# Optimization experiments

Hardware: AMD Instinct MI355X
Metric: run time of the kernel (lower is better)

The kernel has to match this reference:

```python
import jax, jax.numpy as jnp
import numpy as np

N, E, B = 20000, 320000, 64   # nodes, edges, graphs
H, L = 32, 3                  # hidden dim (dim_inner), message passes
HH = H * H
IDX = jnp.array([[0, 1, 2, 3, 4, 5],
                 [1, 6, 7, 8, 9, 10],
                 [2, 7, 11, 12, 13, 14],
                 [3, 8, 12, 15, 16, 17],
                 [4, 9, 13, 16, 18, 19],
                 [5, 10, 14, 17, 19, 20]])


def setup_inputs() -> dict:
    key = jax.random.key(0)
    ks = iter(jax.random.split(key, 40))
    def nrm(shape, s=0.1):
        return jax.random.normal(next(ks), shape, jnp.float32) * s
    inp = {}
    inp['node_attrs'] = jax.random.normal(next(ks), (N, 1), jnp.float32)
    inp['positions'] = jax.random.normal(next(ks), (N, 3), jnp.float32)
    inp['shifts'] = jax.random.normal(next(ks), (E, 3), jnp.float32) * 0.01
    inp['edge_attr'] = jax.random.uniform(next(ks), (E, 1), jnp.float32)
    inp['edge_index'] = jax.random.randint(next(ks), (2, E), 0, N)
    inp['batch_ids'] = jax.random.randint(next(ks), (N,), 0, B)
    # node embedding Linear(1, H)
    inp['embed_W'] = nrm((1, H), 1.0)
    inp['embed_b'] = nrm((H,))
    # per-layer edge MLP: 5 -> H -> H -> H*H (all with bias), plus NNConv bias
    inp['e_W1'] = nrm((L, 5, H), 0.4)
    inp['e_b1'] = nrm((L, H))
    inp['e_W2'] = nrm((L, H, H), 0.15)
    inp['e_b2'] = nrm((L, H))
    inp['e_W3'] = nrm((L, H, HH), 0.15)
    inp['e_b3'] = nrm((L, HH))
    inp['conv_b'] = nrm((L, H))
    # head MLP: H -> 128 -> 64 -> 32 -> 21
    inp['h_W1'] = nrm((H, 128), 0.15)
    inp['h_b1'] = nrm((128,))
    inp['h_W2'] = nrm((128, 64), 0.1)
    inp['h_b2'] = nrm((64,))
    inp['h_W3'] = nrm((64, 32), 0.12)
    inp['h_b3'] = nrm((32,))
    inp['h_W4'] = nrm((32, 21), 0.18)
    inp['h_b4'] = nrm((21,))
    return inp


def reference(node_attrs, positions, shifts, edge_attr, edge_index, batch_ids,
              embed_W, embed_b, e_W1, e_b1, e_W2, e_b2, e_W3, e_b3, conv_b,
              h_W1, h_b1, h_W2, h_b2, h_W3, h_b3, h_W4, h_b4):
    src, dst = edge_index[0], edge_index[1]
    x = node_attrs @ embed_W + embed_b                       # [N, H]
    # get_edge_vectors_and_lengths (MACE convention): receiver - sender + shifts
    vec = positions[dst] - positions[src] + shifts            # [E, 3]
    length = jnp.linalg.norm(vec, axis=-1, keepdims=True)     # [E, 1]
    ef = jnp.concatenate([vec, length, edge_attr], axis=1)    # [E, 5]
    for i in range(L):
        h = jax.nn.relu(ef @ e_W1[i] + e_b1[i])
        h = jax.nn.relu(h @ e_W2[i] + e_b2[i])
        w = jax.nn.relu(h @ e_W3[i] + e_b3[i]).reshape(-1, H, H)  # [E, H, H]
        # NNConv message: x_j @ W_e, aggr='add', root_weight=False, bias=True
        msg = jnp.einsum('eh,ehk->ek', x[src], w)             # [E, H]
        agg = jax.ops.segment_sum(msg, dst, num_segments=N) + conv_b[i]
        x = x + jax.nn.relu(agg)
    # global mean pool over graphs
    ones = jnp.ones((x.shape[0], 1), x.dtype)
    counts = jax.ops.segment_sum(ones, batch_ids, num_segments=B)
    pooled = jax.ops.segment_sum(x, batch_ids, num_segments=B) / jnp.maximum(counts, 1.0)
    h = jax.nn.selu(pooled @ h_W1 + h_b1)
    h = jax.nn.selu(h @ h_W2 + h_b2)
    h = jax.nn.selu(h @ h_W3 + h_b3)
    out = h @ h_W4 + h_b4                                     # [B, 21]
    C = out[:, IDX]                                           # [B, 6, 6]
    return C
```

## Files before the change

kernel.cpp:

```cpp
#include <hip/hip_runtime.h>
#include <hip/hip_bf16.h>

#define N_ 20000
#define E_ 320000
#define B_ 64

typedef __attribute__((ext_vector_type(8))) short short8;
typedef __attribute__((ext_vector_type(4))) float f4;
typedef __attribute__((ext_vector_type(2))) float f2v;
typedef __attribute__((ext_vector_type(4))) unsigned int u4;
typedef __attribute__((ext_vector_type(4))) unsigned short us4;

union U8 { short s[8]; unsigned short us[8]; short8 v; u4 u; };
union F4 { f4 v; f2v h[2]; float f[4]; };

__device__ __forceinline__ float bs2f(unsigned short s) {
    return __uint_as_float(((unsigned int)s) << 16);
}
__device__ __forceinline__ unsigned short f2bs(float f) {
    unsigned int u = __float_as_uint(f);
    unsigned int r = u + 0x7FFFu + ((u >> 16) & 1u);
    return (unsigned short)(r >> 16);
}

#define WAVE_LDS_WAIT() asm volatile("s_waitcnt lgkmcnt(0)" ::: "memory")

#define MFMA_B16(a, b, c) __builtin_amdgcn_mfma_f32_16x16x32_bf16(a, b, c, 0, 0, 0)

__device__ __constant__ int c_IDX[36] = {
    0,1,2,3,4,5, 1,6,7,8,9,10, 2,7,11,12,13,14,
    3,8,12,15,16,17, 4,9,13,16,18,19, 5,10,14,17,19,20};

__global__ __launch_bounds__(256) void k_setup(
    const float* __restrict__ na, const float* __restrict__ eW, const float* __restrict__ eb,
    float* __restrict__ x, int* __restrict__ deg, int* __restrict__ bcnt,
    const float* __restrict__ pos, const float* __restrict__ shifts, const float* __restrict__ eattr,
    const int* __restrict__ eidx, unsigned short* __restrict__ efp,
    const float* __restrict__ w3, unsigned short* __restrict__ w3r,
    const float* __restrict__ w1, const float* __restrict__ w2,
    unsigned short* __restrict__ w1r, unsigned short* __restrict__ w2r,
    const int* __restrict__ batch) {
    int bid = blockIdx.x, t = threadIdx.x;
    if (bid < 2500) {
        int tid = bid * 256 + t;
        int n = tid >> 5, c = tid & 31;
        x[tid] = na[n] * eW[c] + eb[c];
    } else if (bid < 3750) {
        int e = (bid - 2500) * 256 + t;
        int s = eidx[e], d = eidx[E_ + e];
        float vx = pos[d * 3 + 0] - pos[s * 3 + 0] + shifts[e * 3 + 0];
        float vy = pos[d * 3 + 1] - pos[s * 3 + 1] + shifts[e * 3 + 1];
        float vz = pos[d * 3 + 2] - pos[s * 3 + 2] + shifts[e * 3 + 2];
        float ln = sqrtf(vx * vx + vy * vy + vz * vz);
        U8 o;
        o.us[0] = f2bs(vx); o.us[1] = f2bs(vy); o.us[2] = f2bs(vz);
        o.us[3] = f2bs(ln); o.us[4] = f2bs(eattr[e]);
        o.us[5] = 0; o.us[6] = 0; o.us[7] = 0;
        *(u4*)(efp + (size_t)e * 8) = o.u;
        atomicAdd(&deg[d], 1);
    } else if (bid < 3798) {
        int tid = (bid - 3750) * 256 + t;
        int l = tid & 63, t2 = (tid >> 6) & 63, i = tid >> 12;
        int q = l >> 4, m = l & 15;
        U8 o;
        for (int j = 0; j < 8; ++j) {
            int k = q * 8 + j;
            o.us[j] = f2bs(w3[(i * 32 + k) * 1024 + t2 * 16 + m]);
        }
        *(u4*)(w3r + (size_t)tid * 8) = o.u;
    } else if (bid < 3801) {
        int tid = (bid - 3798) * 256 + t;
        bool isw2 = tid >= 384;
        int idx = isw2 ? tid - 384 : tid;
        int i = idx >> 7;
        int tau = (idx >> 6) & 1;
        int l = idx & 63;
        int q = l >> 4, m = l & 15;
        U8 o;
        for (int j = 0; j < 8; ++j) {
            int k = q * 8 + j;
            if (!isw2) o.us[j] = (k < 5) ? f2bs(w1[i * 160 + k * 32 + tau * 16 + m]) : (unsigned short)0;
            else       o.us[j] = f2bs(w2[i * 1024 + k * 32 + tau * 16 + m]);
        }
        unsigned short* dst = (isw2 ? w2r : w1r) + i * 1024 + tau * 512 + l * 8;
        *(u4*)dst = o.u;
    } else {
        __shared__ int s[64];
        if (t < 64) s[t] = 0;
        __syncthreads();
        int n = (bid - 3801) * 256 + t;
        if (n < N_) atomicAdd(&s[batch[n]], 1);
        __syncthreads();
        if (t < 64 && s[t]) atomicAdd(&bcnt[t], s[t]);
    }
}

__global__ __launch_bounds__(1024) void k_scans(const int* __restrict__ deg,
                                                int* __restrict__ off, int* __restrict__ cur,
                                                const int* __restrict__ bcnt,
                                                int* __restrict__ boff, int* __restrict__ bcur) {
    int t = threadIdx.x;
    if (blockIdx.x == 0) {
        __shared__ int sh[1024];
        int base = t * 20;
        int loc[20]; int s = 0;
        for (int k = 0; k < 20; ++k) {
            int i = base + k;
            int v = (i < N_) ? deg[i] : 0;
            loc[k] = s; s += v;
        }
        sh[t] = s;
        __syncthreads();
        for (int d = 1; d < 1024; d <<= 1) {
            int val = (t >= d) ? sh[t - d] : 0;
            __syncthreads();
            sh[t] += val;
            __syncthreads();
        }
        int excl = sh[t] - s;
        for (int k = 0; k < 20; ++k) {
            int i = base + k;
            if (i < N_) { int o = excl + loc[k]; off[i] = o; cur[i] = o; }
        }
        if (t == 1023) off[N_] = sh[1023];
    } else {
        __shared__ int sh[64];
        int v = 0;
        if (t < 64) { v = bcnt[t]; sh[t] = v; }
        __syncthreads();
        for (int d = 1; d < 64; d <<= 1) {
            int val = (t >= d && t < 64) ? sh[t - d] : 0;
            __syncthreads();
            if (t < 64) sh[t] += val;
            __syncthreads();
        }
        if (t < 64) {
            int excl = sh[t] - v;
            boff[t] = excl; bcur[t] = excl;
            if (t == 63) boff[64] = sh[63];
        }
    }
}

__global__ __launch_bounds__(256) void k_fills(const int* __restrict__ eidx,
                                               int* __restrict__ cur, int* __restrict__ rank,
                                               const int* __restrict__ batch,
                                               int* __restrict__ bcur, int* __restrict__ bperm) {
    int bid = blockIdx.x, t = threadIdx.x;
    if (bid < 1250) {
        int e = bid * 256 + t;
        rank[e] = atomicAdd(&cur[eidx[E_ + e]], 1);
    } else {
        int n = (bid - 1250) * 256 + t;
        if (n < N_) {
            int p = atomicAdd(&bcur[batch[n]], 1);
            bperm[p] = n;
        }
    }
}

template <bool STORE>
__global__ __launch_bounds__(256, 6) void k_edge(
    const unsigned short* __restrict__ efp, const int* __restrict__ eidx,
    const int* __restrict__ rank,
    const float* __restrict__ x, float* __restrict__ agg, unsigned short* __restrict__ msg,
    const unsigned short* __restrict__ w1r, const float* __restrict__ b1,
    const unsigned short* __restrict__ w2r, const float* __restrict__ b2,
    const unsigned short* __restrict__ w3r, const float* __restrict__ b3) {
    __shared__ float s_b3[1024];
    __shared__ __align__(16) unsigned short s_h[4][640];
    __shared__ __align__(16) unsigned short s_x[4][2][640];

    const int t = threadIdx.x;
    for (int k = t; k < 1024; k += 256) s_b3[k] = b3[k];

    const int wave = t >> 6, lane = t & 63;
    const int q = lane >> 4, e = lane & 15;
    const int ebase = (blockIdx.x * 4 + wave) * 32;

    for (int g = 0; g < 2; ++g) {
        int srce = eidx[ebase + g * 16 + e];
        const float* xp = x + srce * 32 + q * 8;
        F4 xa, xb2;
        xa.v = *(const f4*)xp;
        xb2.v = *(const f4*)(xp + 4);
        us4 p0, p1;
        for (int r = 0; r < 4; ++r) { p0[r] = f2bs(xa.f[r]); p1[r] = f2bs(xb2.f[r]); }
        unsigned short* dp = &s_x[wave][g][e * 40 + q * 8];
        *(us4*)dp = p0;
        *(us4*)(dp + 4) = p1;
    }

    U8 w1f[2], w2f[2];
    float b1v[2][4], b2v[2][4];
    for (int tau = 0; tau < 2; ++tau) {
        w1f[tau].u = *(const u4*)(w1r + tau * 512 + lane * 8);
        w2f[tau].u = *(const u4*)(w2r + tau * 512 + lane * 8);
        for (int r = 0; r < 4; ++r) {
            b1v[tau][r] = b1[tau * 16 + q * 4 + r];
            b2v[tau][r] = b2[tau * 16 + q * 4 + r];
        }
    }

    const f4 z4 = {0.f, 0.f, 0.f, 0.f};
    short8 h2f[2];

    for (int g = 0; g < 2; ++g) {
        U8 ef;
        if (q == 0) ef.u = *(const u4*)(efp + (size_t)(ebase + g * 16 + e) * 8);
        else { u4 zz = {0u, 0u, 0u, 0u}; ef.u = zz; }

        f4 c0 = MFMA_B16(w1f[0].v, ef.v, z4);
        f4 c1 = MFMA_B16(w1f[1].v, ef.v, z4);
        us4 pk;
        for (int r = 0; r < 4; ++r) pk[r] = f2bs(fmaxf(c0[r] + b1v[0][r], 0.f));
        *(us4*)&s_h[wave][e * 40 + q * 4] = pk;
        for (int r = 0; r < 4; ++r) pk[r] = f2bs(fmaxf(c1[r] + b1v[1][r], 0.f));
        *(us4*)&s_h[wave][e * 40 + 16 + q * 4] = pk;
        WAVE_LDS_WAIT();
        short8 h1f = *(const short8*)&s_h[wave][e * 40 + q * 8];
        c0 = MFMA_B16(w2f[0].v, h1f, z4);
        c1 = MFMA_B16(w2f[1].v, h1f, z4);
        for (int r = 0; r < 4; ++r) pk[r] = f2bs(fmaxf(c0[r] + b2v[0][r], 0.f));
        *(us4*)&s_h[wave][e * 40 + q * 4] = pk;
        for (int r = 0; r < 4; ++r) pk[r] = f2bs(fmaxf(c1[r] + b2v[1][r], 0.f));
        *(us4*)&s_h[wave][e * 40 + 16 + q * 4] = pk;
        WAVE_LDS_WAIT();
        h2f[g] = *(const short8*)&s_h[wave][e * 40 + q * 8];
        WAVE_LDS_WAIT();
    }

    __syncthreads();

    F4 macc[2][2];
    macc[0][0].v = z4; macc[0][1].v = z4; macc[1][0].v = z4; macc[1][1].v = z4;

#pragma unroll 4
    for (int h = 0; h < 32; ++h) {
        short8 a0 = *(const short8*)(w3r + h * 1024 + lane * 8);
        short8 a1 = *(const short8*)(w3r + h * 1024 + 512 + lane * 8);
        f4 ci0 = *(const f4*)&s_b3[h * 32 + q * 4];
        f4 ci1 = *(const f4*)&s_b3[h * 32 + 16 + q * 4];
        for (int g = 0; g < 2; ++g) {
            float xv = bs2f(s_x[wave][g][e * 40 + h]);
            F4 d0, d1, m0, m1;
            d0.v = MFMA_B16(a0, h2f[g], ci0);
            d1.v = MFMA_B16(a1, h2f[g], ci1);
            for (int r = 0; r < 4; ++r) {
                m0.f[r] = fmaxf(d0.f[r], 0.f);
                m1.f[r] = fmaxf(d1.f[r], 0.f);
            }
            f2v xv2 = {xv, xv};
            macc[g][0].h[0] = __builtin_elementwise_fma(m0.h[0], xv2, macc[g][0].h[0]);
            macc[g][0].h[1] = __builtin_elementwise_fma(m0.h[1], xv2, macc[g][0].h[1]);
            macc[g][1].h[0] = __builtin_elementwise_fma(m1.h[0], xv2, macc[g][1].h[0]);
            macc[g][1].h[1] = __builtin_elementwise_fma(m1.h[1], xv2, macc[g][1].h[1]);
        }
    }

    if (STORE) {
        for (int g = 0; g < 2; ++g) {
            int rk = rank[ebase + g * 16 + e];
            unsigned short* mp = msg + (size_t)rk * 32 + q * 4;
            for (int p = 0; p < 2; ++p) {
                us4 pk;
                for (int r = 0; r < 4; ++r) pk[r] = f2bs(macc[g][p].f[r]);
                *(us4*)(mp + p * 16) = pk;
            }
        }
    } else {
        for (int g = 0; g < 2; ++g) {
            int dste = eidx[E_ + ebase + g * 16 + e];
            float* ap = agg + dste * 32 + q * 4;
            for (int p = 0; p < 2; ++p)
                for (int r = 0; r < 4; ++r)
                    atomicAdd(ap + p * 16 + r, macc[g][p].f[r]);
        }
    }
}

__global__ __launch_bounds__(256) void k_gather(const unsigned short* __restrict__ msg,
                                                const int* __restrict__ off,
                                                const float* __restrict__ cb,
                                                float* __restrict__ x) {
    int wave = threadIdx.x >> 6, lane = threadIdx.x & 63;
    int n = blockIdx.x * 4 + wave;
    if (n >= N_) return;
    int j0 = off[n], j1 = off[n + 1];
    const unsigned short* base = msg + (size_t)j0 * 32;
    int nchunk = (j1 - j0) * 4;
    float a[8] = {0.f, 0.f, 0.f, 0.f, 0.f, 0.f, 0.f, 0.f};
    for (int it = lane; it < nchunk; it += 64) {
        u4 v = *(const u4*)(base + it * 8);
        for (int m = 0; m < 4; ++m) {
            unsigned int w = v[m];
            a[2 * m]     += __uint_as_float(w << 16);
            a[2 * m + 1] += __uint_as_float(w & 0xffff0000u);
        }
    }
    for (int d = 4; d < 64; d <<= 1)
        for (int m = 0; m < 8; ++m)
            a[m] += __shfl_xor(a[m], d);
    if (lane < 4) {
        int c0 = lane * 8;
        float* xp = x + n * 32 + c0;
        F4 xa, xb2;
        xa.v = *(const f4*)xp;
        xb2.v = *(const f4*)(xp + 4);
        for (int i = 0; i < 4; ++i) {
            xa.f[i]  += fmaxf(a[i] + cb[c0 + i], 0.f);
            xb2.f[i] += fmaxf(a[4 + i] + cb[c0 + 4 + i], 0.f);
        }
        *(f4*)xp = xa.v;
        *(f4*)(xp + 4) = xb2.v;
    }
}

__device__ __forceinline__ float selu_(float v) {
    return 1.0507009873554805f * (v > 0.f ? v : 1.6732632423543772f * (expf(v) - 1.f));
}

__global__ __launch_bounds__(1024) void k_pool_head(const float* __restrict__ x,
                                                    const int* __restrict__ boff,
                                                    const int* __restrict__ bperm,
                                                    const float* __restrict__ W1, const float* __restrict__ b1,
                                                    const float* __restrict__ W2, const float* __restrict__ b2,
                                                    const float* __restrict__ W3, const float* __restrict__ b3,
                                                    const float* __restrict__ W4, const float* __restrict__ b4,
                                                    float* __restrict__ out) {
    __shared__ float sp[32][32];
    __shared__ float s0[32], s1[128], s2[64], s3[32], s4[21];
    int b = blockIdx.x, t = threadIdx.x, c = t & 31, slot = t >> 5;
    int j0 = boff[b], j1 = boff[b + 1];
    float a = 0.f;
    for (int j = j0 + slot; j < j1; j += 32)
        a += x[bperm[j] * 32 + c];
    sp[slot][c] = a;
    __syncthreads();
    if (t < 32) {
        float s = 0.f;
        for (int k = 0; k < 32; ++k) s += sp[k][t];
        s0[t] = s / fmaxf((float)(j1 - j0), 1.f);
    }
    __syncthreads();
    if (t < 128) {
        float v = b1[t];
        for (int cc = 0; cc < 32; ++cc) v += s0[cc] * W1[cc * 128 + t];
        s1[t] = selu_(v);
    }
    __syncthreads();
    if (t < 64) {
        float v = b2[t];
        for (int cc = 0; cc < 128; ++cc) v += s1[cc] * W2[cc * 64 + t];
        s2[t] = selu_(v);
    }
    __syncthreads();
    if (t < 32) {
        float v = b3[t];
        for (int cc = 0; cc < 64; ++cc) v += s2[cc] * W3[cc * 32 + t];
        s3[t] = selu_(v);
    }
    __syncthreads();
    if (t < 21) {
        float v = b4[t];
        for (int cc = 0; cc < 32; ++cc) v += s3[cc] * W4[cc * 21 + t];
        s4[t] = v;
    }
    __syncthreads();
    if (t < 36) out[b * 36 + t] = s4[c_IDX[t]];
}

__global__ __launch_bounds__(256) void k_init_fb(const float* __restrict__ na,
                                                 const float* __restrict__ eW,
                                                 const float* __restrict__ eb,
                                                 float* __restrict__ x, float* __restrict__ agg) {
    int tid = blockIdx.x * 256 + threadIdx.x;
    int n = tid >> 5, c = tid & 31;
    x[tid] = na[n] * eW[c] + eb[c];
    agg[tid] = 0.f;
}

__global__ __launch_bounds__(256) void k_prep_fb(const float* __restrict__ pos,
                                                 const float* __restrict__ shifts,
                                                 const float* __restrict__ eattr,
                                                 const int* __restrict__ eidx,
                                                 unsigned short* __restrict__ efp) {
    int e = blockIdx.x * 256 + threadIdx.x;
    int s = eidx[e], d = eidx[E_ + e];
    float vx = pos[d * 3 + 0] - pos[s * 3 + 0] + shifts[e * 3 + 0];
    float vy = pos[d * 3 + 1] - pos[s * 3 + 1] + shifts[e * 3 + 1];
    float vz = pos[d * 3 + 2] - pos[s * 3 + 2] + shifts[e * 3 + 2];
    float ln = sqrtf(vx * vx + vy * vy + vz * vz);
    U8 o;
    o.us[0] = f2bs(vx); o.us[1] = f2bs(vy); o.us[2] = f2bs(vz);
    o.us[3] = f2bs(ln); o.us[4] = f2bs(eattr[e]);
    o.us[5] = 0; o.us[6] = 0; o.us[7] = 0;
    *(u4*)(efp + (size_t)e * 8) = o.u;
}

__global__ __launch_bounds__(256) void k_repack_fb(const float* __restrict__ w3,
                                                   unsigned short* __restrict__ w3r,
                                                   const float* __restrict__ w1,
                                                   const float* __restrict__ w2,
                                                   unsigned short* __restrict__ w1r,
                                                   unsigned short* __restrict__ w2r) {
    int tid = blockIdx.x * 256 + threadIdx.x;
    if (tid < 12288) {
        int l = tid & 63, t2 = (tid >> 6) & 63, i = tid >> 12;
        int q = l >> 4, m = l & 15;
        U8 o;
        for (int j = 0; j < 8; ++j) {
            int k = q * 8 + j;
            o.us[j] = f2bs(w3[(i * 32 + k) * 1024 + t2 * 16 + m]);
        }
        *(u4*)(w3r + (size_t)tid * 8) = o.u;
    } else if (tid < 13056) {
        int t2 = tid - 12288;
        bool isw2 = t2 >= 384;
        int idx = isw2 ? t2 - 384 : t2;
        int i = idx >> 7, tau = (idx >> 6) & 1, l = idx & 63;
        int q = l >> 4, m = l & 15;
        U8 o;
        for (int j = 0; j < 8; ++j) {
            int k = q * 8 + j;
            if (!isw2) o.us[j] = (k < 5) ? f2bs(w1[i * 160 + k * 32 + tau * 16 + m]) : (unsigned short)0;
            else       o.us[j] = f2bs(w2[i * 1024 + k * 32 + tau * 16 + m]);
        }
        unsigned short* dst = (isw2 ? w2r : w1r) + i * 1024 + tau * 512 + l * 8;
        *(u4*)dst = o.u;
    }
}

__global__ __launch_bounds__(256) void k_node(float* __restrict__ x, float* __restrict__ agg,
                                              const float* __restrict__ cb) {
    int tid = blockIdx.x * 256 + threadIdx.x;
    int c = tid & 31;
    float a = agg[tid] + cb[c];
    x[tid] += fmaxf(a, 0.f);
    agg[tid] = 0.f;
}

__global__ __launch_bounds__(256) void k_zero_pool(float* __restrict__ pooled, int* __restrict__ cnt) {
    int tid = blockIdx.x * 256 + threadIdx.x;
    if (tid < 2048) pooled[tid] = 0.f;
    else if (tid < 2112) cnt[tid - 2048] = 0;
}

__global__ __launch_bounds__(256) void k_pool(const float* __restrict__ x, const int* __restrict__ batch,
                                              float* __restrict__ pooled, int* __restrict__ cnt) {
    int tid = blockIdx.x * 256 + threadIdx.x;
    int n = tid >> 5, c = tid & 31;
    int b = batch[n];
    atomicAdd(&pooled[b * 32 + c], x[tid]);
    if (c == 0) atomicAdd(&cnt[b], 1);
}

__global__ __launch_bounds__(128) void k_head(const float* __restrict__ pooled, const int* __restrict__ cnt,
                                              const float* __restrict__ W1, const float* __restrict__ b1,
                                              const float* __restrict__ W2, const float* __restrict__ b2,
                                              const float* __restrict__ W3, const float* __restrict__ b3,
                                              const float* __restrict__ W4, const float* __restrict__ b4,
                                              float* __restrict__ out) {
    __shared__ float s0[32], s1[128], s2[64], s3[32], s4[21];
    int b = blockIdx.x, t = threadIdx.x;
    if (t < 32) s0[t] = pooled[b * 32 + t] / fmaxf((float)cnt[b], 1.f);
    __syncthreads();
    {
        float a = b1[t];
        for (int c = 0; c < 32; ++c) a += s0[c] * W1[c * 128 + t];
        s1[t] = selu_(a);
    }
    __syncthreads();
    if (t < 64) {
        float a = b2[t];
        for (int c = 0; c < 128; ++c) a += s1[c] * W2[c * 64 + t];
        s2[t] = selu_(a);
    }
    __syncthreads();
    if (t < 32) {
        float a = b3[t];
        for (int c = 0; c < 64; ++c) a += s2[c] * W3[c * 32 + t];
        s3[t] = selu_(a);
    }
    __syncthreads();
    if (t < 21) {
        float a = b4[t];
        for (int c = 0; c < 32; ++c) a += s3[c] * W4[c * 21 + t];
        s4[t] = a;
    }
    __syncthreads();
    if (t < 36) out[b * 36 + t] = s4[c_IDX[t]];
}

extern "C" void kernel_launch(void* const* d_in, const int* in_sizes, int n_in,
                              void* d_out, int out_size, void* d_ws, size_t ws_size,
                              hipStream_t stream) {
    const float* na     = (const float*)d_in[0];
    const float* pos    = (const float*)d_in[1];
    const float* shifts = (const float*)d_in[2];
    const float* eattr  = (const float*)d_in[3];
    const int*   eidx   = (const int*)d_in[4];
    const int*   batch  = (const int*)d_in[5];
    const float* embW   = (const float*)d_in[6];
    const float* embB   = (const float*)d_in[7];
    const float* eW1    = (const float*)d_in[8];
    const float* eb1    = (const float*)d_in[9];
    const float* eW2    = (const float*)d_in[10];
    const float* eb2    = (const float*)d_in[11];
    const float* eW3    = (const float*)d_in[12];
    const float* eb3    = (const float*)d_in[13];
    const float* cvb    = (const float*)d_in[14];
    const float* hW1    = (const float*)d_in[15];
    const float* hb1    = (const float*)d_in[16];
    const float* hW2    = (const float*)d_in[17];
    const float* hb2    = (const float*)d_in[18];
    const float* hW3    = (const float*)d_in[19];
    const float* hb3    = (const float*)d_in[20];
    const float* hW4    = (const float*)d_in[21];
    const float* hb4    = (const float*)d_in[22];

    const size_t need_csr = (size_t)640000 * 4
                          + (size_t)(20000 + 64 + 20004 + 20000 + 320000 + 68 + 64 + 20000) * 4
                          + ((size_t)E_ * 8 + 98304 + 3072 + 3072 + (size_t)E_ * 32) * 2;

    if (ws_size >= need_csr) {
        char* ws = (char*)d_ws;
        float* x      = (float*)ws;
        int*   deg    = (int*)(x + 640000);
        int*   bcnt   = deg + 20000;
        int*   off    = bcnt + 64;
        int*   cur    = off + 20004;
        int*   rank   = cur + 20000;
        int*   boff   = rank + 320000;
        int*   bcur   = boff + 68;
        int*   bperm  = bcur + 64;
        unsigned short* efp = (unsigned short*)(bperm + 20000);
        unsigned short* w3r = efp + (size_t)E_ * 8;
        unsigned short* w1r = w3r + 98304;
        unsigned short* w2r = w1r + 3072;
        unsigned short* msg = w2r + 3072;

        hipMemsetAsync(deg, 0, (20000 + 64) * sizeof(int), stream);
        k_setup<<<3880, 256, 0, stream>>>(na, embW, embB, x, deg, bcnt,
                                          pos, shifts, eattr, eidx, efp,
                                          eW3, w3r, eW1, eW2, w1r, w2r, batch);
        k_scans<<<2, 1024, 0, stream>>>(deg, off, cur, bcnt, boff, bcur);
        k_fills<<<1329, 256, 0, stream>>>(eidx, cur, rank, batch, bcur, bperm);

        for (int i = 0; i < 3; ++i) {
            k_edge<true><<<2500, 256, 0, stream>>>(efp, eidx, rank, x, nullptr, msg,
                                                   w1r + i * 1024, eb1 + i * 32,
                                                   w2r + i * 1024, eb2 + i * 32,
                                                   w3r + i * 32768, eb3 + i * 1024);
            k_gather<<<5000, 256, 0, stream>>>(msg, off, cvb + i * 32, x);
        }

        k_pool_head<<<64, 1024, 0, stream>>>(x, boff, bperm,
                                             hW1, hb1, hW2, hb2, hW3, hb3, hW4, hb4,
                                             (float*)d_out);
    } else {
        char* ws = (char*)d_ws;
        float* x      = (float*)ws;
        float* agg    = x + 640000;
        float* pooled = agg + 640000;
        int*   cnt    = (int*)(pooled + 2048);
        unsigned short* efp = (unsigned short*)(cnt + 64);
        unsigned short* w3r = efp + (size_t)E_ * 8;
        unsigned short* w1r = w3r + 98304;
        unsigned short* w2r = w1r + 3072;

        k_init_fb<<<2500, 256, 0, stream>>>(na, embW, embB, x, agg);
        k_prep_fb<<<1250, 256, 0, stream>>>(pos, shifts, eattr, eidx, efp);
        k_repack_fb<<<51, 256, 0, stream>>>(eW3, w3r, eW1, eW2, w1r, w2r);
        k_zero_pool<<<9, 256, 0, stream>>>(pooled, cnt);

        for (int i = 0; i < 3; ++i) {
            k_edge<false><<<2500, 256, 0, stream>>>(efp, eidx, nullptr, x, agg, nullptr,
                                                    w1r + i * 1024, eb1 + i * 32,
                                                    w2r + i * 1024, eb2 + i * 32,
                                                    w3r + i * 32768, eb3 + i * 1024);
            k_node<<<2500, 256, 0, stream>>>(x, agg, cvb + i * 32);
        }

        k_pool<<<2500, 256, 0, stream>>>(x, batch, pooled, cnt);
        k_head<<<64, 128, 0, stream>>>(pooled, cnt, hW1, hb1, hW2, hb2, hW3, hb3, hW4, hb4,
                                       (float*)d_out);
    }
}
```

Baseline: 380.9 us.

## Use packed bf16 conversions, wave-shuffle scans, vectorized embed, higher edge occupancy

Replaces the scalar bf16 rounding helper with the packed float2-to-bfloat162 intrinsic throughout the edge MLP, message stores and setup. It also rewrites the prefix scans to use wave shuffles instead of LDS loops with barriers, and vectorizes the node embedding to four outputs per thread, shrinking the setup grid. The edge kernel's launch bounds are raised from 6 to 8 blocks per CU, which may force register spilling in exchange for occupancy.

```diff
diff --git a/kernel.cpp b/kernel.cpp
--- a/kernel.cpp
+++ b/kernel.cpp
@@ -21,6 +21,12 @@
     unsigned int u = __float_as_uint(f);
     unsigned int r = u + 0x7FFFu + ((u >> 16) & 1u);
     return (unsigned short)(r >> 16);
+}
+__device__ __forceinline__ unsigned int pk2(float a, float b) {
+    __hip_bfloat162 h = __float22bfloat162_rn(make_float2(a, b));
+    union { __hip_bfloat162 h2; unsigned int u; } cv;
+    cv.h2 = h;
+    return cv.u;
 }
 
 #define WAVE_LDS_WAIT() asm volatile("s_waitcnt lgkmcnt(0)" ::: "memory")
@@ -41,25 +47,30 @@
     unsigned short* __restrict__ w1r, unsigned short* __restrict__ w2r,
     const int* __restrict__ batch) {
     int bid = blockIdx.x, t = threadIdx.x;
-    if (bid < 2500) {
+    if (bid < 625) {
         int tid = bid * 256 + t;
-        int n = tid >> 5, c = tid & 31;
-        x[tid] = na[n] * eW[c] + eb[c];
-    } else if (bid < 3750) {
-        int e = (bid - 2500) * 256 + t;
+        int base = tid * 4;
+        int n = tid >> 3, c = (tid & 7) * 4;
+        float nv = na[n];
+        F4 o;
+        for (int r = 0; r < 4; ++r) o.f[r] = nv * eW[c + r] + eb[c + r];
+        *(f4*)(x + base) = o.v;
+    } else if (bid < 1875) {
+        int e = (bid - 625) * 256 + t;
         int s = eidx[e], d = eidx[E_ + e];
         float vx = pos[d * 3 + 0] - pos[s * 3 + 0] + shifts[e * 3 + 0];
         float vy = pos[d * 3 + 1] - pos[s * 3 + 1] + shifts[e * 3 + 1];
         float vz = pos[d * 3 + 2] - pos[s * 3 + 2] + shifts[e * 3 + 2];
         float ln = sqrtf(vx * vx + vy * vy + vz * vz);
-        U8 o;
-        o.us[0] = f2bs(vx); o.us[1] = f2bs(vy); o.us[2] = f2bs(vz);
-        o.us[3] = f2bs(ln); o.us[4] = f2bs(eattr[e]);
-        o.us[5] = 0; o.us[6] = 0; o.us[7] = 0;
-        *(u4*)(efp + (size_t)e * 8) = o.u;
+        u4 o;
+        o[0] = pk2(vx, vy);
+        o[1] = pk2(vz, ln);
+        o[2] = pk2(eattr[e], 0.f);
+        o[3] = 0u;
+        *(u4*)(efp + (size_t)e * 8) = o;
         atomicAdd(&deg[d], 1);
-    } else if (bid < 3798) {
-        int tid = (bid - 3750) * 256 + t;
+    } else if (bid < 1923) {
+        int tid = (bid - 1875) * 256 + t;
         int l = tid & 63, t2 = (tid >> 6) & 63, i = tid >> 12;
         int q = l >> 4, m = l & 15;
         U8 o;
@@ -68,8 +79,8 @@
             o.us[j] = f2bs(w3[(i * 32 + k) * 1024 + t2 * 16 + m]);
         }
         *(u4*)(w3r + (size_t)tid * 8) = o.u;
-    } else if (bid < 3801) {
-        int tid = (bid - 3798) * 256 + t;
+    } else if (bid < 1926) {
+        int tid = (bid - 1923) * 256 + t;
         bool isw2 = tid >= 384;
         int idx = isw2 ? tid - 384 : tid;
         int i = idx >> 7;
@@ -88,7 +99,7 @@
         __shared__ int s[64];
         if (t < 64) s[t] = 0;
         __syncthreads();
-        int n = (bid - 3801) * 256 + t;
+        int n = (bid - 1926) * 256 + t;
         if (n < N_) atomicAdd(&s[batch[n]], 1);
         __syncthreads();
         if (t < 64 && s[t]) atomicAdd(&bcnt[t], s[t]);
@@ -101,7 +112,7 @@
                                                 int* __restrict__ boff, int* __restrict__ bcur) {
     int t = threadIdx.x;
     if (blockIdx.x == 0) {
-        __shared__ int sh[1024];
+        __shared__ int shW[16];
         int base = t * 20;
         int loc[20]; int s = 0;
         for (int k = 0; k < 20; ++k) {
@@ -109,35 +120,41 @@
             int v = (i < N_) ? deg[i] : 0;
             loc[k] = s; s += v;
         }
-        sh[t] = s;
+        int lane = t & 63, wv = t >> 6;
+        int v = s;
+        for (int d = 1; d < 64; d <<= 1) {
+            int u = __shfl_up(v, d);
+            if (lane >= d) v += u;
+        }
+        if (lane == 63) shW[wv] = v;
         __syncthreads();
-        for (int d = 1; d < 1024; d <<= 1) {
-            int val = (t >= d) ? sh[t - d] : 0;
-            __syncthreads();
-            sh[t] += val;
-            __syncthreads();
-        }
-        int excl = sh[t] - s;
+        if (wv == 0) {
+            int w = (lane < 16) ? shW[lane] : 0;
+            for (int d = 1; d < 16; d <<= 1) {
+                int u = __shfl_up(w, d);
+                if (lane >= d) w += u;
+            }
+            if (lane < 16) shW[lane] = w;
+        }
+        __syncthreads();
+        int woff = (wv > 0) ? shW[wv - 1] : 0;
+        int incl = v + woff;
+        int excl = incl - s;
         for (int k = 0; k < 20; ++k) {
             int i = base + k;
             if (i < N_) { int o = excl + loc[k]; off[i] = o; cur[i] = o; }
         }
-        if (t == 1023) off[N_] = sh[1023];
+        if (t == 1023) off[N_] = incl;
     } else {
-        __shared__ int sh[64];
-        int v = 0;
-        if (t < 64) { v = bcnt[t]; sh[t] = v; }
-        __syncthreads();
-        for (int d = 1; d < 64; d <<= 1) {
-            int val = (t >= d && t < 64) ? sh[t - d] : 0;
-            __syncthreads();
-            if (t < 64) sh[t] += val;
-            __syncthreads();
-        }
         if (t < 64) {
-            int excl = sh[t] - v;
-            boff[t] = excl; bcur[t] = excl;
-            if (t == 63) boff[64] = sh[63];
+            int v0 = bcnt[t];
+            int v = v0;
+            for (int d = 1; d < 64; d <<= 1) {
+                int u = __shfl_up(v, d);
+                if (t >= d) v += u;
+            }
+            boff[t] = v - v0; bcur[t] = v - v0;
+            if (t == 63) boff[64] = v;
         }
     }
 }
@@ -160,7 +177,7 @@
 }
 
 template <bool STORE>
-__global__ __launch_bounds__(256, 6) void k_edge(
+__global__ __launch_bounds__(256, 8) void k_edge(
     const unsigned short* __restrict__ efp, const int* __restrict__ eidx,
     const int* __restrict__ rank,
     const float* __restrict__ x, float* __restrict__ agg, unsigned short* __restrict__ msg,
@@ -184,11 +201,12 @@
         F4 xa, xb2;
         xa.v = *(const f4*)xp;
         xb2.v = *(const f4*)(xp + 4);
-        us4 p0, p1;
-        for (int r = 0; r < 4; ++r) { p0[r] = f2bs(xa.f[r]); p1[r] = f2bs(xb2.f[r]); }
-        unsigned short* dp = &s_x[wave][g][e * 40 + q * 8];
-        *(us4*)dp = p0;
-        *(us4*)(dp + 4) = p1;
+        u4 P;
+        P[0] = pk2(xa.f[0], xa.f[1]);
+        P[1] = pk2(xa.f[2], xa.f[3]);
+        P[2] = pk2(xb2.f[0], xb2.f[1]);
+        P[3] = pk2(xb2.f[2], xb2.f[3]);
+        *(u4*)&s_x[wave][g][e * 40 + q * 8] = P;
     }
 
     U8 w1f[2], w2f[2];
@@ -212,19 +230,23 @@
 
         f4 c0 = MFMA_B16(w1f[0].v, ef.v, z4);
         f4 c1 = MFMA_B16(w1f[1].v, ef.v, z4);
-        us4 pk;
-        for (int r = 0; r < 4; ++r) pk[r] = f2bs(fmaxf(c0[r] + b1v[0][r], 0.f));
-        *(us4*)&s_h[wave][e * 40 + q * 4] = pk;
-        for (int r = 0; r < 4; ++r) pk[r] = f2bs(fmaxf(c1[r] + b1v[1][r], 0.f));
-        *(us4*)&s_h[wave][e * 40 + 16 + q * 4] = pk;
+        uint2 pkw;
+        pkw.x = pk2(fmaxf(c0[0] + b1v[0][0], 0.f), fmaxf(c0[1] + b1v[0][1], 0.f));
+        pkw.y = pk2(fmaxf(c0[2] + b1v[0][2], 0.f), fmaxf(c0[3] + b1v[0][3], 0.f));
+        *(uint2*)&s_h[wave][e * 40 + q * 4] = pkw;
+        pkw.x = pk2(fmaxf(c1[0] + b1v[1][0], 0.f), fmaxf(c1[1] + b1v[1][1], 0.f));
+        pkw.y = pk2(fmaxf(c1[2] + b1v[1][2], 0.f), fmaxf(c1[3] + b1v[1][3], 0.f));
+        *(uint2*)&s_h[wave][e * 40 + 16 + q * 4] = pkw;
         WAVE_LDS_WAIT();
         short8 h1f = *(const short8*)&s_h[wave][e * 40 + q * 8];
         c0 = MFMA_B16(w2f[0].v, h1f, z4);
         c1 = MFMA_B16(w2f[1].v, h1f, z4);
-        for (int r = 0; r < 4; ++r) pk[r] = f2bs(fmaxf(c0[r] + b2v[0][r], 0.f));
-        *(us4*)&s_h[wave][e * 40 + q * 4] = pk;
-        for (int r = 0; r < 4; ++r) pk[r] = f2bs(fmaxf(c1[r] + b2v[1][r], 0.f));
-        *(us4*)&s_h[wave][e * 40 + 16 + q * 4] = pk;
+        pkw.x = pk2(fmaxf(c0[0] + b2v[0][0], 0.f), fmaxf(c0[1] + b2v[0][1], 0.f));
+        pkw.y = pk2(fmaxf(c0[2] + b2v[0][2], 0.f), fmaxf(c0[3] + b2v[0][3], 0.f));
+        *(uint2*)&s_h[wave][e * 40 + q * 4] = pkw;
+        pkw.x = pk2(fmaxf(c1[0] + b2v[1][0], 0.f), fmaxf(c1[1] + b2v[1][1], 0.f));
+        pkw.y = pk2(fmaxf(c1[2] + b2v[1][2], 0.f), fmaxf(c1[3] + b2v[1][3], 0.f));
+        *(uint2*)&s_h[wave][e * 40 + 16 + q * 4] = pkw;
         WAVE_LDS_WAIT();
         h2f[g] = *(const short8*)&s_h[wave][e * 40 + q * 8];
         WAVE_LDS_WAIT();
@@ -263,9 +285,10 @@
             int rk = rank[ebase + g * 16 + e];
             unsigned short* mp = msg + (size_t)rk * 32 + q * 4;
             for (int p = 0; p < 2; ++p) {
-                us4 pk;
-                for (int r = 0; r < 4; ++r) pk[r] = f2bs(macc[g][p].f[r]);
-                *(us4*)(mp + p * 16) = pk;
+                uint2 m;
+                m.x = pk2(macc[g][p].f[0], macc[g][p].f[1]);
+                m.y = pk2(macc[g][p].f[2], macc[g][p].f[3]);
+                *(uint2*)(mp + p * 16) = m;
             }
         }
     } else {
@@ -391,11 +414,12 @@
     float vy = pos[d * 3 + 1] - pos[s * 3 + 1] + shifts[e * 3 + 1];
     float vz = pos[d * 3 + 2] - pos[s * 3 + 2] + shifts[e * 3 + 2];
     float ln = sqrtf(vx * vx + vy * vy + vz * vz);
-    U8 o;
-    o.us[0] = f2bs(vx); o.us[1] = f2bs(vy); o.us[2] = f2bs(vz);
-    o.us[3] = f2bs(ln); o.us[4] = f2bs(eattr[e]);
-    o.us[5] = 0; o.us[6] = 0; o.us[7] = 0;
-    *(u4*)(efp + (size_t)e * 8) = o.u;
+    u4 o;
+    o[0] = pk2(vx, vy);
+    o[1] = pk2(vz, ln);
+    o[2] = pk2(eattr[e], 0.f);
+    o[3] = 0u;
+    *(u4*)(efp + (size_t)e * 8) = o;
 }
 
 __global__ __launch_bounds__(256) void k_repack_fb(const float* __restrict__ w3,
@@ -541,7 +565,7 @@
         unsigned short* msg = w2r + 3072;
 
         hipMemsetAsync(deg, 0, (20000 + 64) * sizeof(int), stream);
-        k_setup<<<3880, 256, 0, stream>>>(na, embW, embB, x, deg, bcnt,
+        k_setup<<<2005, 256, 0, stream>>>(na, embW, embB, x, deg, bcnt,
                                           pos, shifts, eattr, eidx, efp,
                                           eW3, w3r, eW1, eW2, w1r, w2r, batch);
         k_scans<<<2, 1024, 0, stream>>>(deg, off, cur, bcnt, boff, bcur);
```

After: 377.8 us. No clear change (-0.8%).
